# Kernel optimization log

Hardware: AMD Instinct MI355X
Metric: run time of the kernel (lower is better)

Reference implementation:

```python
import math
import jax, jax.numpy as jnp
import numpy as np

S = 2048
HIDDEN = 5120
H = 16              # num_local_heads (128 global heads / TP=8)
NOPE, ROPE, V = 128, 64, 128
QK = NOPE + ROPE    # 192 (module pads to 256; zero-pad is a mathematical no-op)
QLORA, KVLORA = 1536, 512
EPS = 1e-6
BASE, FACTOR = 10000.0, 40.0
BETA_FAST, BETA_SLOW = 32.0, 1.0
ORIG_MAX = 4096
MSCALE = MSCALE_ALL = 0.707


def _yarn_get_mscale(scale, mscale):
    if scale <= 1:
        return 1.0
    return 0.1 * mscale * math.log(scale) + 1.0


SCALING = QK ** -0.5 * _yarn_get_mscale(FACTOR, MSCALE_ALL) ** 2
COS_SIN_MSCALE = _yarn_get_mscale(FACTOR, MSCALE) / _yarn_get_mscale(FACTOR, MSCALE_ALL)


def _yarn_inv_freq():
    half = ROPE // 2
    i = np.arange(half, dtype=np.float64)
    pos_freqs = BASE ** (2.0 * i / ROPE)
    inv_extra = 1.0 / pos_freqs
    inv_interp = 1.0 / (FACTOR * pos_freqs)

    def corr_dim(n_rot):
        return ROPE * math.log(ORIG_MAX / (n_rot * 2 * math.pi)) / (2 * math.log(BASE))

    low = max(math.floor(corr_dim(BETA_FAST)), 0)
    high = min(math.ceil(corr_dim(BETA_SLOW)), ROPE - 1)
    ramp = np.clip((i - low) / max(high - low, 1e-3), 0.0, 1.0)
    inv_freq_mask = 1.0 - ramp  # 1 -> extrapolation, 0 -> interpolation
    inv_freq = inv_interp * (1.0 - inv_freq_mask) + inv_extra * inv_freq_mask
    return jnp.asarray(inv_freq, dtype=jnp.float32)


INV_FREQ = _yarn_inv_freq()  # [ROPE/2]


def _apply_rope(x, cos, sin):
    # non-neox (interleaved pairs): x [S, heads, ROPE], cos/sin [S, ROPE/2]
    x1 = x[..., 0::2]
    x2 = x[..., 1::2]
    c = cos[:, None, :]
    s = sin[:, None, :]
    o1 = x1 * c - x2 * s
    o2 = x2 * c + x1 * s
    return jnp.stack([o1, o2], axis=-1).reshape(x.shape)


def _rms_norm(x, w):
    var = jnp.mean(x.astype(jnp.float32) ** 2, axis=-1, keepdims=True)
    return (x.astype(jnp.float32) * jax.lax.rsqrt(var + EPS)).astype(x.dtype) * w


def setup_inputs() -> dict:
    key = jax.random.key(0)
    ks = jax.random.split(key, 8)
    sd = 0.02
    return {
        'positions': jnp.arange(S, dtype=jnp.int64 if jax.config.jax_enable_x64 else jnp.int32),
        'hidden_states': jax.random.normal(ks[0], (S, HIDDEN), jnp.float32),
        'w_q_a': jax.random.normal(ks[1], (HIDDEN, QLORA), jnp.float32) * sd,
        'q_a_ln_w': jnp.ones((QLORA,), jnp.float32),
        'w_q_b': jax.random.normal(ks[2], (QLORA, H * QK), jnp.float32) * sd,
        'w_kv_a': jax.random.normal(ks[3], (HIDDEN, KVLORA + ROPE), jnp.float32) * sd,
        'kv_a_ln_w': jnp.ones((KVLORA,), jnp.float32),
        'w_kv_b': jax.random.normal(ks[4], (KVLORA, H * (NOPE + V)), jnp.float32) * sd,
        'w_o': jax.random.normal(ks[5], (H * V, HIDDEN), jnp.float32) * sd,
    }


def reference(positions, hidden_states, w_q_a, q_a_ln_w, w_q_b, w_kv_a, kv_a_ln_w, w_kv_b, w_o):
    # Q low-rank path: q_a_proj -> RMSNorm -> q_b_proj
    q = hidden_states @ w_q_a                       # [S, QLORA]
    q = _rms_norm(q, q_a_ln_w)
    q = (q @ w_q_b).reshape(S, H, QK)               # [S, H, 192]
    q_nope, q_pe = q[..., :NOPE], q[..., NOPE:]

    # KV latent path: shared MQA latent + decoupled rope key
    latent = hidden_states @ w_kv_a                 # [S, KVLORA+ROPE]
    kv_a = _rms_norm(latent[:, :KVLORA], kv_a_ln_w)
    k_pe = latent[:, None, KVLORA:]                 # [S, 1, ROPE]
    kv = (kv_a @ w_kv_b).reshape(S, H, NOPE + V)
    k_nope, v = kv[..., :NOPE], kv[..., NOPE:]

    # partial (decoupled) yarn RoPE on the 64-dim rope slice
    freqs = positions.astype(jnp.float32)[:, None] * INV_FREQ[None, :]
    cos = jnp.cos(freqs) * COS_SIN_MSCALE
    sin = jnp.sin(freqs) * COS_SIN_MSCALE
    q_pe = _apply_rope(q_pe, cos, sin)
    k_pe = _apply_rope(k_pe, cos, sin)

    qf = jnp.concatenate([q_nope, q_pe], axis=-1)   # [S, H, 192]
    kf = jnp.concatenate([k_nope, jnp.broadcast_to(k_pe, (S, H, ROPE))], axis=-1)

    # causal paged-attention prefill; zero-padding head dims to 256 is a no-op
    scores = jnp.einsum('qhd,khd->hqk', qf, kf) * SCALING  # [H, S, S]
    causal = jnp.tril(jnp.ones((S, S), dtype=bool))
    scores = jnp.where(causal[None], scores, -jnp.inf)
    probs = jax.nn.softmax(scores, axis=-1)
    attn = jnp.einsum('hqk,khd->qhd', probs, v).reshape(S, H * V)
    return attn @ w_o                               # [S, HIDDEN]
```

## Files before the change

### kernel.cpp

```cpp
#include <hip/hip_runtime.h>
#include <math.h>

typedef unsigned short u16;
typedef unsigned int u32;
typedef __attribute__((ext_vector_type(4))) float f32x4;
typedef __attribute__((ext_vector_type(8))) unsigned short u16x8;
typedef __attribute__((ext_vector_type(4))) unsigned short u16x4;
typedef __attribute__((ext_vector_type(8))) __bf16 bf16x8;

#define DEV __device__ __forceinline__

constexpr int S = 2048;
constexpr int HIDDEN = 5120;
constexpr int H = 16;
constexpr int NOPE = 128, ROPE_D = 64, VD = 128;
constexpr int QKD = NOPE + ROPE_D;
constexpr int QLORA = 1536, KVLORA = 512;
constexpr int KVA_N = KVLORA + ROPE_D;
constexpr float SCALING = 0.11472134f;

DEV u16 f2b(float f) {
  u32 u = __builtin_bit_cast(u32, f);
  u32 r = u + 0x7FFFu + ((u >> 16) & 1u);
  return (u16)(r >> 16);
}
DEV float b2f(u16 h) { return __builtin_bit_cast(float, (u32)h << 16); }

DEV void store_out(float* p, float v) { *p = v; }
DEV void store_out(u16* p, float v) { *p = f2b(v); }

DEV void gload_lds16(const u16* g, u16* l) {
  auto* gp = (const __attribute__((address_space(1))) u16*)g;
  auto* lp = (__attribute__((address_space(3))) u16*)l;
  __builtin_amdgcn_global_load_lds(gp, lp, 16, 0, 0);
}

#define SWZ(row, col) ((col) ^ (((row) & 7) << 3))

DEV void transpose_tile(const float* __restrict__ in, u16* __restrict__ out,
                        int R, int C, int c0, int r0, int tid, float (*tl)[33]) {
  int tx = tid & 31, ty = tid >> 5;
  for (int r = ty; r < 32; r += 8)
    tl[r][tx] = in[(size_t)(r0 + r) * C + c0 + tx];
  __syncthreads();
  for (int r = ty; r < 32; r += 8)
    out[(size_t)(c0 + r) * R + r0 + tx] = f2b(tl[tx][r]);
}

__global__ __launch_bounds__(256) void k_prep(const float* __restrict__ hidden, u16* __restrict__ hs_bf,
                                              const float* __restrict__ w_q_a, u16* __restrict__ bt_qa,
                                              const float* __restrict__ w_kv_a, u16* __restrict__ bt_kva,
                                              const float* __restrict__ w_q_b, u16* __restrict__ bt_qb,
                                              const float* __restrict__ w_kv_b, u16* __restrict__ bt_kvb,
                                              float* __restrict__ cs, float* __restrict__ sn) {
  __shared__ float tl[32][33];
  int b = blockIdx.x, tid = threadIdx.x;
  if (b < 10240) {
    int i = (b * 256 + tid) * 4;
    f32x4 v = *reinterpret_cast<const f32x4*>(hidden + i);
    u16x4 o;
    o[0] = f2b(v[0]); o[1] = f2b(v[1]); o[2] = f2b(v[2]); o[3] = f2b(v[3]);
    *reinterpret_cast<u16x4*>(hs_bf + i) = o;
    return;
  }
  b -= 10240;
  if (b < 7680) {
    transpose_tile(w_q_a, bt_qa, HIDDEN, QLORA, (b % 48) * 32, (b / 48) * 32, tid, tl);
    return;
  }
  b -= 7680;
  if (b < 2880) {
    transpose_tile(w_kv_a, bt_kva, HIDDEN, KVA_N, (b % 18) * 32, (b / 18) * 32, tid, tl);
    return;
  }
  b -= 2880;
  if (b < 4608) {
    transpose_tile(w_q_b, bt_qb, QLORA, H * QKD, (b % 96) * 32, (b / 96) * 32, tid, tl);
    return;
  }
  b -= 4608;
  if (b < 2048) {
    transpose_tile(w_kv_b, bt_kvb, KVLORA, H * 256, (b % 128) * 32, (b / 128) * 32, tid, tl);
    return;
  }
  b -= 2048;
  int idx = b * 256 + tid;
  int s = idx >> 5, j = idx & 31;
  double pf = pow(10000.0, (double)j / 32.0);
  double inv_extra = 1.0 / pf;
  double inv_interp = 1.0 / (40.0 * pf);
  double twopi = 6.283185307179586476925286766559;
  double lnb2 = 2.0 * log(10000.0);
  double lowd = floor(64.0 * log(4096.0 / (32.0 * twopi)) / lnb2);
  if (lowd < 0.0) lowd = 0.0;
  double highd = ceil(64.0 * log(4096.0 / twopi) / lnb2);
  if (highd > 63.0) highd = 63.0;
  double denom = highd - lowd;
  if (denom < 0.001) denom = 0.001;
  double ramp = ((double)j - lowd) / denom;
  ramp = ramp < 0.0 ? 0.0 : (ramp > 1.0 ? 1.0 : ramp);
  float invf = (float)(inv_interp * ramp + inv_extra * (1.0 - ramp));
  float fr = (float)s * invf;
  cs[idx] = cosf(fr);
  sn[idx] = sinf(fr);
}

DEV void gemm_core(u16* Al, u16* Bl, const u16* __restrict__ A,
                   const u16* __restrict__ BT,
                   int Kstride, int Klen, int mbase, int nbase, f32x4 (*acc)[4]) {
  const int tid = threadIdx.x;
  const int lane = tid & 63, wave = tid >> 6;
  const int wr = wave >> 1, wc = wave & 1;
  const int lr = lane & 15, lk = lane >> 4;
  const int srow = wave * 32 + (lane >> 2);
  const int skoff = (((lane & 3) ^ ((lane >> 3) & 3))) * 8;
  const int swlk8 = (lk ^ ((lr >> 1) & 3)) * 8;
  const u16* aptr = A + (size_t)(mbase + srow) * Kstride + skoff;
  const u16* bptr = BT + (size_t)(nbase + srow) * Kstride + skoff;
  u16* alw = Al + wave * (32 * 32);
  u16* blw = Bl + wave * (32 * 32);

  auto STAGE = [&](int b, int kk) {
    gload_lds16(aptr + kk, alw + b * 4096);
    gload_lds16(aptr + (size_t)16 * Kstride + kk, alw + b * 4096 + 16 * 32);
    gload_lds16(bptr + kk, blw + b * 4096);
    gload_lds16(bptr + (size_t)16 * Kstride + kk, blw + b * 4096 + 16 * 32);
  };

#pragma unroll
  for (int mf = 0; mf < 4; ++mf)
#pragma unroll
    for (int nf = 0; nf < 4; ++nf) acc[mf][nf] = {0.f, 0.f, 0.f, 0.f};

  const int nt = Klen >> 5;
  STAGE(0, 0);
  STAGE(1, 32);
  for (int t = 0; t < nt; ++t) {
    const int cur = t & 1;
    if (t + 1 < nt)
      asm volatile("s_waitcnt vmcnt(4)" ::: "memory");
    else
      asm volatile("s_waitcnt vmcnt(0)" ::: "memory");
    __builtin_amdgcn_s_barrier();
    const u16* Ac = Al + cur * 4096;
    const u16* Bc = Bl + cur * 4096;
    bf16x8 af[4], bfr[4];
#pragma unroll
    for (int mf = 0; mf < 4; ++mf)
      af[mf] = *reinterpret_cast<const bf16x8*>(Ac + (wr * 64 + mf * 16 + lr) * 32 + swlk8);
#pragma unroll
    for (int nf = 0; nf < 4; ++nf)
      bfr[nf] = *reinterpret_cast<const bf16x8*>(Bc + (wc * 64 + nf * 16 + lr) * 32 + swlk8);
#pragma unroll
    for (int mf = 0; mf < 4; ++mf)
#pragma unroll
      for (int nf = 0; nf < 4; ++nf)
        acc[mf][nf] = __builtin_amdgcn_mfma_f32_16x16x32_bf16(af[mf], bfr[nf], acc[mf][nf], 0, 0, 0);
    __builtin_amdgcn_s_barrier();
    if (t + 2 < nt) STAGE(cur, (t + 2) * 32);
  }
}

template <typename OutT>
DEV void gemm_epilogue(f32x4 (*acc)[4], OutT* __restrict__ C, int N, int mbase, int nbase) {
  const int lane = threadIdx.x & 63, wave = threadIdx.x >> 6;
  const int wr = wave >> 1, wc = wave & 1;
  const int lr = lane & 15, lk = lane >> 4;
#pragma unroll
  for (int mf = 0; mf < 4; ++mf)
#pragma unroll
    for (int nf = 0; nf < 4; ++nf) {
      int col = nbase + wc * 64 + nf * 16 + lr;
      if (col < N) {
#pragma unroll
        for (int r = 0; r < 4; ++r) {
          int row = mbase + wr * 64 + mf * 16 + lk * 4 + r;
          store_out(&C[(size_t)row * N + col], acc[mf][nf][r]);
        }
      }
    }
}

__global__ __launch_bounds__(256) void k_gemm_out(const u16* __restrict__ A,
                                                  const u16* __restrict__ BT,
                                                  float* __restrict__ C) {
  __shared__ u16 Al[2 * 128 * 32];
  __shared__ u16 Bl[2 * 128 * 32];
  int id = blockIdx.x;
  int row = id & 15, col = id >> 4;
  f32x4 acc[4][4];
  gemm_core(Al, Bl, A, BT, H * VD, H * VD, row * 128, col * 128, acc);
  gemm_epilogue(acc, C, HIDDEN, row * 128, col * 128);
}

__global__ __launch_bounds__(256) void k_gemm_up(const u16* __restrict__ Aq, const u16* __restrict__ Bq,
                                                 const u16* __restrict__ Akv, const u16* __restrict__ Bkv,
                                                 const float* __restrict__ cs, const float* __restrict__ sn,
                                                 u16* __restrict__ qf, u16* __restrict__ kf,
                                                 u16* __restrict__ vt) {
  __shared__ u16 Al[2 * 128 * 32];
  __shared__ u16 Bl[2 * 128 * 32];
  int id = blockIdx.x;
  int rowb = id & 15, col = id >> 4;
  const int mbase = rowb * 128;
  const int lane = threadIdx.x & 63, wave = threadIdx.x >> 6;
  const int wr = wave >> 1, wc = wave & 1;
  const int lr = lane & 15, lk = lane >> 4;
  f32x4 acc[4][4];
  if (col < 24) {
    const int nbase = col * 128;
    gemm_core(Al, Bl, Aq, Bq, QLORA, QLORA, mbase, nbase, acc);
#pragma unroll
    for (int nf = 0; nf < 4; ++nf) {
      int colb = nbase + wc * 64 + nf * 16;
      int h = colb / 192;
      int db = colb - h * 192;
      size_t qoff = (size_t)h * S * QKD;
      if (db < NOPE) {
#pragma unroll
        for (int mf = 0; mf < 4; ++mf)
#pragma unroll
          for (int r = 0; r < 4; ++r) {
            int row = mbase + wr * 64 + mf * 16 + lk * 4 + r;
            qf[qoff + (size_t)row * QKD + db + lr] = f2b(acc[mf][nf][r]);
          }
      } else {
        int jj = (db - NOPE + lr) >> 1;
        bool odd = lr & 1;
#pragma unroll
        for (int mf = 0; mf < 4; ++mf)
#pragma unroll
          for (int r = 0; r < 4; ++r) {
            int row = mbase + wr * 64 + mf * 16 + lk * 4 + r;
            float val = acc[mf][nf][r];
            float part = __shfl_xor(val, 1);
            float c = cs[row * 32 + jj], s = sn[row * 32 + jj];
            float o = odd ? (val * c + part * s) : (val * c - part * s);
            qf[qoff + (size_t)row * QKD + db + lr] = f2b(o);
          }
      }
    }
  } else {
    const int nbase = (col - 24) * 128;
    gemm_core(Al, Bl, Akv, Bkv, KVLORA, KVLORA, mbase, nbase, acc);
#pragma unroll
    for (int nf = 0; nf < 4; ++nf) {
      int colb = nbase + wc * 64 + nf * 16;
      int h = colb >> 8;
      int db = colb & 255;
      if (db < NOPE) {
        size_t koff = (size_t)h * S * QKD;
#pragma unroll
        for (int mf = 0; mf < 4; ++mf)
#pragma unroll
          for (int r = 0; r < 4; ++r) {
            int row = mbase + wr * 64 + mf * 16 + lk * 4 + r;
            kf[koff + (size_t)row * QKD + db + lr] = f2b(acc[mf][nf][r]);
          }
      } else {
        int vtrow = h * VD + db - NOPE + lr;
#pragma unroll
        for (int mf = 0; mf < 4; ++mf) {
          int row0 = mbase + wr * 64 + mf * 16 + lk * 4;
          u16x4 pk;
          pk[0] = f2b(acc[mf][nf][0]); pk[1] = f2b(acc[mf][nf][1]);
          pk[2] = f2b(acc[mf][nf][2]); pk[3] = f2b(acc[mf][nf][3]);
          *reinterpret_cast<u16x4*>(&vt[(size_t)vtrow * S + row0]) = pk;
        }
      }
    }
  }
}

__global__ __launch_bounds__(256) void k_gemm_dp(const u16* __restrict__ A,
                                                 const u16* __restrict__ Bq,
                                                 const u16* __restrict__ Bkv,
                                                 float* __restrict__ q0, float* __restrict__ q1,
                                                 float* __restrict__ l0, float* __restrict__ l1) {
  __shared__ u16 Al[2 * 128 * 32];
  __shared__ u16 Bl[2 * 128 * 32];
  constexpr int KH = HIDDEN / 2;
  int id = blockIdx.x;
  int split = id >= 272;
  int u = id - split * 272;
  int row = u & 15, colt = u >> 4;
  const u16* As = A + split * KH;
  f32x4 acc[4][4];
  if (colt < 12) {
    gemm_core(Al, Bl, As, Bq + split * KH, HIDDEN, KH, row * 128, colt * 128, acc);
    gemm_epilogue(acc, split ? q1 : q0, QLORA, row * 128, colt * 128);
  } else {
    gemm_core(Al, Bl, As, Bkv + split * KH, HIDDEN, KH, row * 128, (colt - 12) * 128, acc);
    gemm_epilogue(acc, split ? l1 : l0, KVA_N, row * 128, (colt - 12) * 128);
  }
}

DEV void rmsnorm2_row(const float* __restrict__ x0, const float* __restrict__ x1,
                      const float* __restrict__ w, u16* __restrict__ y,
                      int ncols, int instride, int row, int tid, float* red) {
  const float* xr0 = x0 + (size_t)row * instride;
  const float* xr1 = x1 + (size_t)row * instride;
  float ss = 0.f;
  for (int i = tid * 4; i < ncols; i += 1024) {
    f32x4 a = *reinterpret_cast<const f32x4*>(xr0 + i);
    f32x4 b = *reinterpret_cast<const f32x4*>(xr1 + i);
    f32x4 v = a + b;
    ss += v[0] * v[0] + v[1] * v[1] + v[2] * v[2] + v[3] * v[3];
  }
  for (int off = 32; off > 0; off >>= 1) ss += __shfl_down(ss, off);
  if ((tid & 63) == 0) red[tid >> 6] = ss;
  __syncthreads();
  ss = red[0] + red[1] + red[2] + red[3];
  float sc = rsqrtf(ss / (float)ncols + 1e-6f);
  u16* yr = y + (size_t)row * ncols;
  for (int i = tid * 4; i < ncols; i += 1024) {
    f32x4 a = *reinterpret_cast<const f32x4*>(xr0 + i);
    f32x4 b = *reinterpret_cast<const f32x4*>(xr1 + i);
    f32x4 v = a + b;
    u16x4 o;
    o[0] = f2b(v[0] * sc * w[i]);
    o[1] = f2b(v[1] * sc * w[i + 1]);
    o[2] = f2b(v[2] * sc * w[i + 2]);
    o[3] = f2b(v[3] * sc * w[i + 3]);
    *reinterpret_cast<u16x4*>(yr + i) = o;
  }
}

__global__ __launch_bounds__(256) void k_mid(const float* __restrict__ q0, const float* __restrict__ q1,
                                             const float* __restrict__ qw, u16* __restrict__ q_ln,
                                             const float* __restrict__ l0, const float* __restrict__ l1,
                                             const float* __restrict__ kw, u16* __restrict__ kv_ln,
                                             const float* __restrict__ w_o, u16* __restrict__ bt_o,
                                             const float* __restrict__ cs, const float* __restrict__ sn,
                                             u16* __restrict__ kf) {
  __shared__ float red[4];
  __shared__ float tl[32][33];
  int b = blockIdx.x, tid = threadIdx.x;
  if (b < 2048) {
    rmsnorm2_row(q0, q1, qw, q_ln, QLORA, QLORA, b, tid, red);
    return;
  }
  if (b < 4096) {
    rmsnorm2_row(l0, l1, kw, kv_ln, KVLORA, KVA_N, b - 2048, tid, red);
    return;
  }
  if (b < 14336) {
    int u = b - 4096;
    transpose_tile(w_o, bt_o, H * VD, HIDDEN, (u % 160) * 32, (u / 160) * 32, tid, tl);
    return;
  }
  int s = b - 14336;
  for (int idx = tid; idx < H * 32; idx += 256) {
    int h = idx >> 5, j = idx & 31;
    float c = cs[s * 32 + j], si = sn[s * 32 + j];
    float k1 = l0[(size_t)s * KVA_N + KVLORA + 2 * j] + l1[(size_t)s * KVA_N + KVLORA + 2 * j];
    float k2 = l0[(size_t)s * KVA_N + KVLORA + 2 * j + 1] + l1[(size_t)s * KVA_N + KVLORA + 2 * j + 1];
    kf[((size_t)h * S + s) * QKD + NOPE + 2 * j] = f2b(k1 * c - k2 * si);
    kf[((size_t)h * S + s) * QKD + NOPE + 2 * j + 1] = f2b(k2 * c + k1 * si);
  }
}

__global__ __launch_bounds__(256) void k_attn(const u16* __restrict__ qf,
                                              const u16* __restrict__ kf,
                                              const u16* __restrict__ vt,
                                              u16* __restrict__ attn) {
  const int bidx = blockIdx.x;
  const int j = bidx & 31;
  const int h = bidx >> 5;
  const int qt = (h < 8) ? j : 31 - j;
  const int qbase = qt * 64;
  const int tid = threadIdx.x, wave = tid >> 6, lane = tid & 63;
  const int lr = lane & 15, lk = lane >> 4;
  __shared__ u16 Kl[64][192];
  __shared__ u16 Vl[128][64];
  __shared__ u16 Pl[4][16][64];

  int krow_[6], kofs_[6], vrow_[4], vofs_[4];
#pragma unroll
  for (int i = 0; i < 6; ++i) { int c = tid + i * 256; krow_[i] = c / 24; kofs_[i] = (c % 24) * 8; }
#pragma unroll
  for (int i = 0; i < 4; ++i) { int c = tid + i * 256; vrow_[i] = c >> 3; vofs_[i] = (c & 7) * 8; }
  const u16* kfh = kf + (size_t)h * S * QKD;
  const u16* vth = vt + (size_t)h * VD * S;

  bf16x8 qfrag[6];
  const u16* qrow = qf + ((size_t)h * S + qbase + wave * 16 + lr) * QKD;
#pragma unroll
  for (int d = 0; d < 6; ++d)
    qfrag[d] = *reinterpret_cast<const bf16x8*>(qrow + d * 32 + lk * 8);

  u16x8 kreg[6], vreg[4];
#pragma unroll
  for (int i = 0; i < 6; ++i)
    kreg[i] = *reinterpret_cast<const u16x8*>(kfh + (size_t)krow_[i] * QKD + kofs_[i]);
#pragma unroll
  for (int i = 0; i < 4; ++i)
    vreg[i] = *reinterpret_cast<const u16x8*>(vth + (size_t)vrow_[i] * S + vofs_[i]);

  f32x4 o[8];
#pragma unroll
  for (int f = 0; f < 8; ++f) o[f] = {0.f, 0.f, 0.f, 0.f};
  float m_[4] = {-__builtin_inff(), -__builtin_inff(), -__builtin_inff(), -__builtin_inff()};
  float l_[4] = {0.f, 0.f, 0.f, 0.f};

  const int ktiles = qt + 1;
  for (int kt = 0; kt < ktiles; ++kt) {
    const int kbase = kt * 64;
    __builtin_amdgcn_s_barrier();
#pragma unroll
    for (int i = 0; i < 6; ++i)
      *reinterpret_cast<u16x8*>(&Kl[krow_[i]][SWZ(krow_[i], kofs_[i])]) = kreg[i];
#pragma unroll
    for (int i = 0; i < 4; ++i)
      *reinterpret_cast<u16x8*>(&Vl[vrow_[i]][SWZ(vrow_[i], vofs_[i])]) = vreg[i];
    if (kt + 1 < ktiles) {
      const int nb = kbase + 64;
#pragma unroll
      for (int i = 0; i < 6; ++i)
        kreg[i] = *reinterpret_cast<const u16x8*>(kfh + (size_t)(nb + krow_[i]) * QKD + kofs_[i]);
#pragma unroll
      for (int i = 0; i < 4; ++i)
        vreg[i] = *reinterpret_cast<const u16x8*>(vth + (size_t)vrow_[i] * S + nb + vofs_[i]);
    }
    asm volatile("s_waitcnt lgkmcnt(0)" ::: "memory");
    __builtin_amdgcn_s_barrier();

    f32x4 sacc[4];
#pragma unroll
    for (int nf = 0; nf < 4; ++nf) sacc[nf] = {0.f, 0.f, 0.f, 0.f};
    __builtin_amdgcn_s_setprio(1);
#pragma unroll
    for (int nf = 0; nf < 4; ++nf)
#pragma unroll
      for (int dk = 0; dk < 6; ++dk) {
        int krow = nf * 16 + lr;
        bf16x8 b = *reinterpret_cast<const bf16x8*>(&Kl[krow][SWZ(krow, dk * 32 + lk * 8)]);
        sacc[nf] = __builtin_amdgcn_mfma_f32_16x16x32_bf16(qfrag[dk], b, sacc[nf], 0, 0, 0);
      }
    __builtin_amdgcn_s_setprio(0);

    float sv[4][4];
    float rowmax[4] = {-__builtin_inff(), -__builtin_inff(), -__builtin_inff(), -__builtin_inff()};
#pragma unroll
    for (int nf = 0; nf < 4; ++nf) {
      int kcol = kbase + nf * 16 + lr;
#pragma unroll
      for (int r = 0; r < 4; ++r) {
        float v = sacc[nf][r] * SCALING;
        int qrow_g = qbase + wave * 16 + lk * 4 + r;
        if (kcol > qrow_g) v = -__builtin_inff();
        sv[nf][r] = v;
        rowmax[r] = fmaxf(rowmax[r], v);
      }
    }
#pragma unroll
    for (int r = 0; r < 4; ++r) {
#pragma unroll
      for (int off = 1; off < 16; off <<= 1)
        rowmax[r] = fmaxf(rowmax[r], __shfl_xor(rowmax[r], off));
    }
    float needm = fmaxf(fmaxf(rowmax[0] - m_[0], rowmax[1] - m_[1]),
                        fmaxf(rowmax[2] - m_[2], rowmax[3] - m_[3]));
    if (!__all(needm <= 8.0f)) {
#pragma unroll
      for (int r = 0; r < 4; ++r) {
        float mn = fmaxf(m_[r], rowmax[r]);
        float alpha = __expf(m_[r] - mn);
        m_[r] = mn;
        l_[r] *= alpha;
#pragma unroll
        for (int f = 0; f < 8; ++f) o[f][r] *= alpha;
      }
    }
    float rowsum[4] = {0.f, 0.f, 0.f, 0.f};
#pragma unroll
    for (int nf = 0; nf < 4; ++nf)
#pragma unroll
      for (int r = 0; r < 4; ++r) {
        float p = __expf(sv[nf][r] - m_[r]);
        sv[nf][r] = p;
        rowsum[r] += p;
      }
#pragma unroll
    for (int r = 0; r < 4; ++r) {
#pragma unroll
      for (int off = 1; off < 16; off <<= 1) rowsum[r] += __shfl_xor(rowsum[r], off);
      l_[r] += rowsum[r];
    }
#pragma unroll
    for (int nf = 0; nf < 4; ++nf)
#pragma unroll
      for (int r = 0; r < 4; ++r) {
        int prow = lk * 4 + r;
        Pl[wave][prow][SWZ(prow, nf * 16 + lr)] = f2b(sv[nf][r]);
      }

    __builtin_amdgcn_s_setprio(1);
#pragma unroll
    for (int kk = 0; kk < 2; ++kk) {
      bf16x8 pa = *reinterpret_cast<const bf16x8*>(&Pl[wave][lr][SWZ(lr, kk * 32 + lk * 8)]);
#pragma unroll
      for (int f = 0; f < 8; ++f) {
        int vrow = f * 16 + lr;
        bf16x8 b = *reinterpret_cast<const bf16x8*>(&Vl[vrow][SWZ(vrow, kk * 32 + lk * 8)]);
        o[f] = __builtin_amdgcn_mfma_f32_16x16x32_bf16(pa, b, o[f], 0, 0, 0);
      }
    }
    __builtin_amdgcn_s_setprio(0);
  }

#pragma unroll
  for (int f = 0; f < 8; ++f)
#pragma unroll
    for (int r = 0; r < 4; ++r) {
      int row = qbase + wave * 16 + lk * 4 + r;
      float val = o[f][r] / l_[r];
      attn[(size_t)row * (H * VD) + h * VD + f * 16 + lr] = f2b(val);
    }
}

extern "C" void kernel_launch(void* const* d_in, const int* in_sizes, int n_in,
                              void* d_out, int out_size, void* d_ws, size_t ws_size,
                              hipStream_t stream) {
  (void)in_sizes; (void)n_in; (void)out_size; (void)ws_size;
  const float* hidden    = (const float*)d_in[1];
  const float* w_q_a     = (const float*)d_in[2];
  const float* q_a_ln_w  = (const float*)d_in[3];
  const float* w_q_b     = (const float*)d_in[4];
  const float* w_kv_a    = (const float*)d_in[5];
  const float* kv_a_ln_w = (const float*)d_in[6];
  const float* w_kv_b    = (const float*)d_in[7];
  const float* w_o       = (const float*)d_in[8];
  float* out = (float*)d_out;

  char* ws = (char*)d_ws;
  size_t off = 0;
  auto alloc = [&](size_t bytes) {
    size_t o = off;
    off += (bytes + 255) & ~(size_t)255;
    return o;
  };
  constexpr int KVA_PAD = 640;
  size_t o_hs    = alloc((size_t)S * HIDDEN * 2);
  size_t o_btqa  = alloc((size_t)QLORA * HIDDEN * 2);
  size_t o_btkva = alloc((size_t)KVA_PAD * HIDDEN * 2);
  size_t o_btqb  = alloc((size_t)(H * QKD) * QLORA * 2);
  size_t o_btkvb = alloc((size_t)(H * 256) * KVLORA * 2);
  size_t o_qlat0 = alloc((size_t)S * QLORA * 4);
  size_t o_qlat1 = alloc((size_t)S * QLORA * 4);
  size_t o_lat0  = alloc((size_t)S * KVA_N * 4);
  size_t o_lat1  = alloc((size_t)S * KVA_N * 4);
  size_t o_qln   = alloc((size_t)S * QLORA * 2);
  size_t o_kvln  = alloc((size_t)S * KVLORA * 2);
  size_t o_kf    = alloc((size_t)H * S * QKD * 2);
  size_t o_vt    = alloc((size_t)H * VD * S * 2);
  size_t o_cs    = alloc((size_t)S * 32 * 4);
  size_t o_sn    = alloc((size_t)S * 32 * 4);

  u16* hs_bf  = (u16*)(ws + o_hs);
  u16* bt_qa  = (u16*)(ws + o_btqa);
  u16* bt_kva = (u16*)(ws + o_btkva);
  u16* bt_qb  = (u16*)(ws + o_btqb);
  u16* bt_kvb = (u16*)(ws + o_btkvb);
  float* q_lat0 = (float*)(ws + o_qlat0);
  float* q_lat1 = (float*)(ws + o_qlat1);
  float* lat0   = (float*)(ws + o_lat0);
  float* lat1   = (float*)(ws + o_lat1);
  u16* q_ln  = (u16*)(ws + o_qln);
  u16* kv_ln = (u16*)(ws + o_kvln);
  u16* kf    = (u16*)(ws + o_kf);
  u16* vt    = (u16*)(ws + o_vt);
  float* cs = (float*)(ws + o_cs);
  float* sn = (float*)(ws + o_sn);
  u16* qf   = (u16*)(ws + o_hs);
  u16* bt_o = (u16*)(ws + o_btqa);
  u16* attn = (u16*)(ws + o_qlat0);

  k_prep<<<dim3(27712), dim3(256), 0, stream>>>(hidden, hs_bf, w_q_a, bt_qa,
                                                w_kv_a, bt_kva, w_q_b, bt_qb,
                                                w_kv_b, bt_kvb, cs, sn);

  k_gemm_dp<<<dim3(544), dim3(256), 0, stream>>>(hs_bf, bt_qa, bt_kva,
                                                 q_lat0, q_lat1, lat0, lat1);

  k_mid<<<dim3(16384), dim3(256), 0, stream>>>(q_lat0, q_lat1, q_a_ln_w, q_ln,
                                               lat0, lat1, kv_a_ln_w, kv_ln,
                                               w_o, bt_o, cs, sn, kf);

  k_gemm_up<<<dim3(896), dim3(256), 0, stream>>>(q_ln, bt_qb, kv_ln, bt_kvb,
                                                 cs, sn, qf, kf, vt);

  k_attn<<<dim3(512), dim3(256), 0, stream>>>(qf, kf, vt, attn);

  k_gemm_out<<<dim3(640), dim3(256), 0, stream>>>(attn, bt_o, out);
}
```

Before: 315.3 us.

## Transpose attention MFMA operands so P stays in registers, drop LDS round-trip

```diff
diff --git a/kernel.cpp b/kernel.cpp
--- a/kernel.cpp
+++ b/kernel.cpp
@@ -6,6 +6,7 @@
 typedef __attribute__((ext_vector_type(4))) float f32x4;
 typedef __attribute__((ext_vector_type(8))) unsigned short u16x8;
 typedef __attribute__((ext_vector_type(4))) unsigned short u16x4;
+typedef __attribute__((ext_vector_type(4))) unsigned int u32x4;
 typedef __attribute__((ext_vector_type(8))) __bf16 bf16x8;
 
 #define DEV __device__ __forceinline__
@@ -373,7 +374,6 @@
   const int lr = lane & 15, lk = lane >> 4;
   __shared__ u16 Kl[64][192];
   __shared__ u16 Vl[128][64];
-  __shared__ u16 Pl[4][16][64];
 
   int krow_[6], kofs_[6], vrow_[4], vofs_[4];
 #pragma unroll
@@ -400,8 +400,9 @@
   f32x4 o[8];
 #pragma unroll
   for (int f = 0; f < 8; ++f) o[f] = {0.f, 0.f, 0.f, 0.f};
-  float m_[4] = {-__builtin_inff(), -__builtin_inff(), -__builtin_inff(), -__builtin_inff()};
-  float l_[4] = {0.f, 0.f, 0.f, 0.f};
+  float m_ = -__builtin_inff();
+  float l_ = 0.f;
+  const int qrow_g = qbase + wave * 16 + lr;
 
   const int ktiles = qt + 1;
   for (int kt = 0; kt < ktiles; ++kt) {
@@ -434,89 +435,89 @@
 #pragma unroll
       for (int dk = 0; dk < 6; ++dk) {
         int krow = nf * 16 + lr;
-        bf16x8 b = *reinterpret_cast<const bf16x8*>(&Kl[krow][SWZ(krow, dk * 32 + lk * 8)]);
-        sacc[nf] = __builtin_amdgcn_mfma_f32_16x16x32_bf16(qfrag[dk], b, sacc[nf], 0, 0, 0);
+        bf16x8 a = *reinterpret_cast<const bf16x8*>(&Kl[krow][SWZ(krow, dk * 32 + lk * 8)]);
+        sacc[nf] = __builtin_amdgcn_mfma_f32_16x16x32_bf16(a, qfrag[dk], sacc[nf], 0, 0, 0);
       }
     __builtin_amdgcn_s_setprio(0);
 
-    float sv[4][4];
-    float rowmax[4] = {-__builtin_inff(), -__builtin_inff(), -__builtin_inff(), -__builtin_inff()};
-#pragma unroll
-    for (int nf = 0; nf < 4; ++nf) {
-      int kcol = kbase + nf * 16 + lr;
+    float p[4][4];
+    float rowmax = -__builtin_inff();
+#pragma unroll
+    for (int nf = 0; nf < 4; ++nf)
 #pragma unroll
       for (int r = 0; r < 4; ++r) {
         float v = sacc[nf][r] * SCALING;
-        int qrow_g = qbase + wave * 16 + lk * 4 + r;
+        int kcol = kbase + nf * 16 + lk * 4 + r;
         if (kcol > qrow_g) v = -__builtin_inff();
-        sv[nf][r] = v;
-        rowmax[r] = fmaxf(rowmax[r], v);
-      }
-    }
-#pragma unroll
-    for (int r = 0; r < 4; ++r) {
-#pragma unroll
-      for (int off = 1; off < 16; off <<= 1)
-        rowmax[r] = fmaxf(rowmax[r], __shfl_xor(rowmax[r], off));
-    }
-    float needm = fmaxf(fmaxf(rowmax[0] - m_[0], rowmax[1] - m_[1]),
-                        fmaxf(rowmax[2] - m_[2], rowmax[3] - m_[3]));
-    if (!__all(needm <= 8.0f)) {
+        p[nf][r] = v;
+        rowmax = fmaxf(rowmax, v);
+      }
+    rowmax = fmaxf(rowmax, __shfl_xor(rowmax, 16));
+    rowmax = fmaxf(rowmax, __shfl_xor(rowmax, 32));
+
+    if (!__all(rowmax - m_ <= 8.0f)) {
+      float mn = fmaxf(m_, rowmax);
+      float alpha = __expf(m_ - mn);
+      m_ = mn;
+      l_ *= alpha;
+#pragma unroll
+      for (int f = 0; f < 8; ++f)
+#pragma unroll
+        for (int r = 0; r < 4; ++r) o[f][r] *= alpha;
+    }
+    float rowsum = 0.f;
+#pragma unroll
+    for (int nf = 0; nf < 4; ++nf)
 #pragma unroll
       for (int r = 0; r < 4; ++r) {
-        float mn = fmaxf(m_[r], rowmax[r]);
-        float alpha = __expf(m_[r] - mn);
-        m_[r] = mn;
-        l_[r] *= alpha;
-#pragma unroll
-        for (int f = 0; f < 8; ++f) o[f][r] *= alpha;
-      }
-    }
-    float rowsum[4] = {0.f, 0.f, 0.f, 0.f};
-#pragma unroll
-    for (int nf = 0; nf < 4; ++nf)
-#pragma unroll
-      for (int r = 0; r < 4; ++r) {
-        float p = __expf(sv[nf][r] - m_[r]);
-        sv[nf][r] = p;
-        rowsum[r] += p;
-      }
-#pragma unroll
-    for (int r = 0; r < 4; ++r) {
-#pragma unroll
-      for (int off = 1; off < 16; off <<= 1) rowsum[r] += __shfl_xor(rowsum[r], off);
-      l_[r] += rowsum[r];
-    }
-#pragma unroll
-    for (int nf = 0; nf < 4; ++nf)
-#pragma unroll
-      for (int r = 0; r < 4; ++r) {
-        int prow = lk * 4 + r;
-        Pl[wave][prow][SWZ(prow, nf * 16 + lr)] = f2b(sv[nf][r]);
-      }
-
+        float e = __expf(p[nf][r] - m_);
+        p[nf][r] = e;
+        rowsum += e;
+      }
+    rowsum += __shfl_xor(rowsum, 16);
+    rowsum += __shfl_xor(rowsum, 32);
+    l_ += rowsum;
+
+    u32 P2[4][2];
+#pragma unroll
+    for (int nf = 0; nf < 4; ++nf) {
+#pragma unroll
+      for (int w = 0; w < 2; ++w)
+        P2[nf][w] = (u32)f2b(p[nf][2 * w]) | ((u32)f2b(p[nf][2 * w + 1]) << 16);
+    }
+
+    const int srcA = lr + 32 * (lk & 1);
+    const int srcB = srcA + 16;
+    const bool lo = (lk < 2);
     __builtin_amdgcn_s_setprio(1);
 #pragma unroll
     for (int kk = 0; kk < 2; ++kk) {
-      bf16x8 pa = *reinterpret_cast<const bf16x8*>(&Pl[wave][lr][SWZ(lr, kk * 32 + lk * 8)]);
+      u32 a0 = __shfl((int)P2[2 * kk][0], srcA), a1 = __shfl((int)P2[2 * kk][1], srcA);
+      u32 a2 = __shfl((int)P2[2 * kk][0], srcB), a3 = __shfl((int)P2[2 * kk][1], srcB);
+      u32 b0 = __shfl((int)P2[2 * kk + 1][0], srcA), b1 = __shfl((int)P2[2 * kk + 1][1], srcA);
+      u32 b2 = __shfl((int)P2[2 * kk + 1][0], srcB), b3 = __shfl((int)P2[2 * kk + 1][1], srcB);
+      u32x4 wsel;
+      wsel[0] = lo ? a0 : b0; wsel[1] = lo ? a1 : b1;
+      wsel[2] = lo ? a2 : b2; wsel[3] = lo ? a3 : b3;
+      bf16x8 pvB = __builtin_bit_cast(bf16x8, wsel);
 #pragma unroll
       for (int f = 0; f < 8; ++f) {
         int vrow = f * 16 + lr;
-        bf16x8 b = *reinterpret_cast<const bf16x8*>(&Vl[vrow][SWZ(vrow, kk * 32 + lk * 8)]);
-        o[f] = __builtin_amdgcn_mfma_f32_16x16x32_bf16(pa, b, o[f], 0, 0, 0);
+        bf16x8 a = *reinterpret_cast<const bf16x8*>(&Vl[vrow][SWZ(vrow, kk * 32 + lk * 8)]);
+        o[f] = __builtin_amdgcn_mfma_f32_16x16x32_bf16(a, pvB, o[f], 0, 0, 0);
       }
     }
     __builtin_amdgcn_s_setprio(0);
   }
 
-#pragma unroll
-  for (int f = 0; f < 8; ++f)
-#pragma unroll
-    for (int r = 0; r < 4; ++r) {
-      int row = qbase + wave * 16 + lk * 4 + r;
-      float val = o[f][r] / l_[r];
-      attn[(size_t)row * (H * VD) + h * VD + f * 16 + lr] = f2b(val);
-    }
+  float inv_l = 1.0f / l_;
+#pragma unroll
+  for (int f = 0; f < 8; ++f) {
+    u16x4 pk;
+#pragma unroll
+    for (int r = 0; r < 4; ++r) pk[r] = f2b(o[f][r] * inv_l);
+    *reinterpret_cast<u16x4*>(&attn[(size_t)qrow_g * (H * VD) + h * VD + f * 16 + 4 * lk]) = pk;
+  }
 }
 
 extern "C" void kernel_launch(void* const* d_in, const int* in_sizes, int n_in,
```

New measurement: 313.3 us (median of 2 runs). Within noise of the previous version (-0.6%).
